# Kernel optimization log

Measured on AMD Instinct MI355X. Metric: run time of the kernel, lower is better.

## Reference

```python
import jax, jax.numpy as jnp
import numpy as np

H = 512  # hidden_dim
F = 512  # feat_vec_dim
N_LEAVES = 2048
BATCH = 8


def _tree_indices(n_leaves, batch_size):
    """Complete-binary-tree forest, nodes numbered bottom-up per tree:
    leaves 0..L-1, then L..L+L/2-1, ..., root last. Returns per-non-leaf-layer
    son/fa global index arrays (concatenated over the batch of trees)."""
    npt = 2 * n_leaves - 1  # nodes per tree
    levels = []
    start, size = 0, n_leaves
    while size >= 1:
        levels.append((start, size))
        start += size
        size //= 2
    offs = np.arange(batch_size) * npt
    def idx(l):
        s, sz = levels[l]
        return jnp.asarray((offs[:, None] + np.arange(s, s + sz)[None, :]).reshape(-1))
    n_layers = len(levels) - 1  # number of non-leaf layers (11 here)
    son = [idx(l) for l in range(n_layers)]
    fa = [idx(l + 1) for l in range(n_layers)]
    return son, fa, npt * batch_size, n_layers


def setup_inputs() -> dict:
    key = jax.random.key(0)
    ks = jax.random.split(key, 24)
    n_total = (2 * N_LEAVES - 1) * BATCH  # 32760
    s = 1.0 / np.sqrt(F)
    mk = lambda k: jax.random.normal(k, (H, F), dtype=jnp.float32) * s
    vk = lambda k: jax.random.normal(k, (H,), dtype=jnp.float32) * 0.02
    return {
        "feat_vec": jax.random.normal(ks[0], (n_total, F), dtype=jnp.float32),
        "Wh": mk(ks[1]), "Wz": mk(ks[2]), "Wr": mk(ks[3]),
        "Uh": mk(ks[4]), "Uz": mk(ks[5]), "bUz": vk(ks[6]),
        "Ur": mk(ks[7]), "bUr": vk(ks[8]),
        "Whd": mk(ks[9]), "Wzd": mk(ks[10]), "Wrd": mk(ks[11]),
        "Uhd": mk(ks[12]), "Uzd": mk(ks[13]), "bUzd": vk(ks[14]),
        "Urd": mk(ks[15]), "bUrd": vk(ks[16]),
        "W1": mk(ks[17]), "b1": jax.random.normal(ks[18], (F,), dtype=jnp.float32) * 0.02,
        "W2": mk(ks[19]), "b2": jax.random.normal(ks[20], (F,), dtype=jnp.float32) * 0.02,
        "n_leaves": N_LEAVES,
        "batch_size": BATCH,
    }


def reference(feat_vec, Wh, Wz, Wr, Uh, Uz, bUz, Ur, bUr,
              Whd, Wzd, Wrd, Uhd, Uzd, bUzd, Urd, bUrd,
              W1, b1, W2, b2, n_leaves, batch_size):
    son, fa, n_total, n_layers = _tree_indices(int(n_leaves), int(batch_size))
    sig, tanh = jax.nn.sigmoid, jnp.tanh

    # ---- bottom-up tree GRU ----
    h = jnp.zeros((n_total, H), dtype=feat_vec.dtype)
    # leaves: h = (1-z) * tanh(Wh x), z = sigmoid(Wz x)
    x0 = feat_vec[son[0]]
    z0 = sig(x0 @ Wz.T)
    h = h.at[son[0]].set((1.0 - z0) * tanh(x0 @ Wh.T))
    for l in range(n_layers):
        # A_T_sub @ h_son == sum of each father's two contiguous children
        h_son = h[son[l]]
        h_sum = h_son.reshape(-1, 2, H).sum(axis=1)
        x = feat_vec[fa[l]]
        z = sig(x @ Wz.T + h_sum @ Uz.T + bUz)
        r = sig(x @ Wr.T + h_sum @ Ur.T + bUr)
        cand = tanh(x @ Wh.T + (r * h_sum) @ Uh.T)
        h = h.at[fa[l]].set(z * h_sum + (1.0 - z) * cand)

    # ---- top-down tree GRU ----
    hd = jnp.zeros((n_total, H), dtype=feat_vec.dtype)
    roots = fa[n_layers - 1]
    hd = hd.at[roots].set(h[roots])
    for l in range(n_layers - 1, -1, -1):
        # A_sub @ hd_fa == each son gathers its (single) father's state
        h_fa = jnp.repeat(hd[fa[l]], 2, axis=0)
        x = feat_vec[son[l]]
        zd = sig(x @ Wzd.T + h_fa @ Uzd.T + bUzd)
        rd = sig(x @ Wrd.T + h_fa @ Urd.T + bUrd)
        cand = tanh(x @ Whd.T + (rd * h_fa) @ Uhd.T)
        hd = hd.at[son[l]].set(zd * h_fa + (1.0 - zd) * cand)

    # out = FFN1(h) + FFN2(hd)
    return h @ W1.T + b1 + hd @ W2.T + b2
```

## Files before the change

kernel.cpp:

```cpp
#include <hip/hip_runtime.h>
#include <hip/hip_bf16.h>
#include <cmath>
#include <cstdint>

#define NPT 4095
#define NT  32760
#define FD  512

using bf16 = __hip_bfloat16;
using bf8v = __attribute__((ext_vector_type(8))) short;
using us8v = __attribute__((ext_vector_type(8))) unsigned short;
using f4v  = __attribute__((ext_vector_type(4))) float;

__device__ __forceinline__ float b2f(bf16 x){ return __bfloat162float(x); }
__device__ __forceinline__ bf16  f2b(float x){ return __float2bfloat16(x); }
__device__ __forceinline__ float us2f(unsigned short u){ union{unsigned int i; float f;} v; v.i = ((unsigned)u)<<16; return v.f; }
__device__ __forceinline__ unsigned short f2us(float f){ union{bf16 b; unsigned short u;} v; v.b = __float2bfloat16(f); return v.u; }

__device__ __forceinline__ float fast_sig(float x){
  float e = __builtin_amdgcn_exp2f(-1.4426950408889634f * x);
  return __builtin_amdgcn_rcpf(1.f + e);
}
__device__ __forceinline__ float fast_tanh(float x){
  float ax = fabsf(x);
  float e = __builtin_amdgcn_exp2f(-2.885390081777927f * ax);
  float r = (1.f - e) * __builtin_amdgcn_rcpf(1.f + e);
  return copysignf(r, x);
}

__device__ __forceinline__ void gload_lds16(const bf16* g, bf16* l){
  __builtin_amdgcn_global_load_lds(
    (const __attribute__((address_space(1))) unsigned int*)g,
    (__attribute__((address_space(3))) unsigned int*)l, 16, 0, 0);
}


__global__ void cvt_b16(bf16* __restrict__ dst, const float* __restrict__ src, int n8){
  int e = blockIdx.x*256 + threadIdx.x;
  if (e >= n8) return;
  const float4* s = (const float4*)(src + (size_t)e*8);
  float4 a = s[0], b = s[1];
  us8v o = { f2us(a.x), f2us(a.y), f2us(a.z), f2us(a.w),
             f2us(b.x), f2us(b.y), f2us(b.z), f2us(b.w) };
  *(us8v*)(dst + (size_t)e*8) = o;
}

struct PackArgs { const float* s[16]; bf16* d[16]; int dk[16]; int ro[16]; int co[16]; };
__global__ void pack_all(PackArgs pa){
  int idx = blockIdx.x >> 7;
  int e = (blockIdx.x & 127)*256 + threadIdx.x;
  int r = e >> 6, c8 = e & 63;
  const float4* s = (const float4*)(pa.s[idx] + (size_t)r*512 + c8*8);
  float4 a = s[0], b = s[1];
  us8v o = { f2us(a.x), f2us(a.y), f2us(a.z), f2us(a.w),
             f2us(b.x), f2us(b.y), f2us(b.z), f2us(b.w) };
  *(us8v*)(pa.d[idx] + (size_t)(pa.ro[idx] + r)*pa.dk[idx] + pa.co[idx] + c8*8) = o;
}

__global__ void roots_k(bf16* __restrict__ hd, bf16* __restrict__ sA, const bf16* __restrict__ h){
  int e = blockIdx.x*256 + threadIdx.x;
  int t = e >> 6, c8 = e & 63;
  size_t off = ((size_t)t*NPT + 4094)*FD + c8*8;
  us8v v = *(const us8v*)(h + off);
  *(us8v*)(hd + off) = v;
  *(us8v*)(sA + (size_t)(2*t)*FD + c8*8) = v;
  *(us8v*)(sA + (size_t)(2*t+1)*FD + c8*8) = v;
}

__device__ __forceinline__ void epi4(
    const f4v& a, int rbase, int n, int M, int mode,
    const float* __restrict__ bias0, const float* __restrict__ bias1,
    const bf16* __restrict__ zb, const bf16* __restrict__ sb,
    const bf16* __restrict__ xw,
    bf16* __restrict__ o0, bf16* __restrict__ o1,
    bf16* __restrict__ hO, float* __restrict__ outF,
    int o_start, int o_log2, bf16* __restrict__ sN, int smode)
{
  if (rbase >= M) return;
  const int omask = (1 << o_log2) - 1;
  if (mode == 1){
    #pragma unroll
    for (int i = 0; i < 4; ++i){
      int row = rbase + i; if (row >= M) break;
      int tree = row >> o_log2, pos = row & omask;
      float v = a[i] + b2f(xw[((size_t)tree*NPT + o_start + pos)*1024 + n]);
      if (n < 512){
        o0[(size_t)row*FD + n] = f2b(fast_sig(v + bias0[n]));
      } else {
        float r = fast_sig(v + bias1[n-512]);
        size_t off = (size_t)row*FD + (n-512);
        o1[off] = f2b(r * b2f(sb[off]));
      }
    }
  } else {
    float hv[4];
    #pragma unroll
    for (int i = 0; i < 4; ++i){
      int row = rbase + i;
      if (row >= M){ hv[i] = 0.f; continue; }
      float c = fast_tanh(a[i]);
      size_t off = (size_t)row*FD + n;
      float z = b2f(zb[off]);
      float s = b2f(sb[off]);
      float h = z*s + (1.f - z)*c;
      hv[i] = h;
      int tree = row >> o_log2, pos = row & omask;
      hO[((size_t)tree*NPT + o_start + pos)*FD + n] = f2b(h);
    }
    if (smode == 1){
      if (rbase + 1 < M) sN[(size_t)(rbase>>1)*FD + n] = f2b(hv[0] + hv[1]);
      if (rbase + 3 < M) sN[(size_t)((rbase>>1) + 1)*FD + n] = f2b(hv[2] + hv[3]);
    } else if (smode == 2){
      #pragma unroll
      for (int i = 0; i < 4; ++i){
        int row = rbase + i; if (row >= M) break;
        bf16 hb = f2b(hv[i]);
        sN[(size_t)(2*row)*FD + n] = hb;
        sN[(size_t)(2*row+1)*FD + n] = hb;
      }
    }
  }
}

#define CPAD 132
__global__ __launch_bounds__(256) void gemm_big(
    const bf16* __restrict__ A0, const bf16* __restrict__ A1,
    const bf16* __restrict__ Wp, int M, int K, int ldb,
    int a_start, int a_log2, int o_start, int o_log2,
    const float* __restrict__ bias0, const float* __restrict__ bias1,
    const bf16* __restrict__ zb, const bf16* __restrict__ sb,
    const bf16* __restrict__ xw,
    bf16* __restrict__ o0, bf16* __restrict__ o1,
    bf16* __restrict__ hO, float* __restrict__ outF,
    bf16* __restrict__ sN, int smode, int mode)
{
  __shared__ __align__(16) char smemraw[64*CPAD*4];
  bf16* As = (bf16*)smemraw;
  bf16* Bs = As + 128*64;
  float* Cf = (float*)smemraw;

  const int t = threadIdx.x, lane = t & 63, wid = t >> 6;
  const int wr = wid >> 1, wc = wid & 1;
  const int lr = lane & 15, quad = lane >> 4;

  const int gx = gridDim.x, gy = gridDim.y;
  int nwg = gx * gy;
  int id = blockIdx.y * gx + blockIdx.x;
  int q = nwg >> 3, r8 = nwg & 7;
  int xcd = id & 7, jj = id >> 3;
  int wg = (xcd < r8 ? xcd*(q+1) : r8*(q+1) + (xcd - r8)*q) + jj;
  const int m_blk = (wg / gy) * 128, n_blk = (wg % gy) * 128;

  const int Mm1 = M - 1;
  const int amask = (1 << a_log2) - 1;
  const int wbase = (t & ~63);

  const bf16* a0p[4]; const bf16* a1p[4]; const bf16* bp[4];
  #pragma unroll
  for (int p = 0; p < 4; ++p){
    int c = p*256 + t;
    int rl = c >> 3, slot = c & 7;
    int g = slot ^ (rl & 7);
    int r = m_blk + rl; if (r > Mm1) r = Mm1;
    int tr = r >> a_log2, po = r & amask;
    a0p[p] = A0 + ((size_t)tr*NPT + a_start + po)*FD + g*8;
    a1p[p] = A1 + (size_t)r*FD + g*8;
    bp[p]  = Wp + (size_t)(n_blk + rl)*ldb + g*8;
  }

  f4v acc[4][4] = {};

  for (int k0 = 0; k0 < K; k0 += 64){
    #pragma unroll
    for (int p = 0; p < 4; ++p){
      const bf16* src = (k0 < 512) ? (a0p[p] + k0) : (a1p[p] + (k0 - 512));
      gload_lds16(src, &As[(size_t)(p*256 + wbase)*8]);
    }
    #pragma unroll
    for (int p = 0; p < 4; ++p)
      gload_lds16(bp[p] + k0, &Bs[(size_t)(p*256 + wbase)*8]);
    __syncthreads();

    #pragma unroll
    for (int kh = 0; kh < 2; ++kh){
      int cidx = kh*4 + quad;
      bf8v af[4], bv[4];
      #pragma unroll
      for (int i = 0; i < 4; ++i){
        int ra = wr*64 + i*16 + lr;
        af[i] = *(const bf8v*)&As[ra*64 + ((cidx ^ (ra & 7))*8)];
        int rb = wc*64 + i*16 + lr;
        bv[i] = *(const bf8v*)&Bs[rb*64 + ((cidx ^ (rb & 7))*8)];
      }
      #pragma unroll
      for (int i = 0; i < 4; ++i)
        #pragma unroll
        for (int j = 0; j < 4; ++j)
          acc[i][j] = __builtin_amdgcn_mfma_f32_16x16x32_bf16(af[i], bv[j], acc[i][j], 0, 0, 0);
    }
    __syncthreads();
  }

  const int omask = (1 << o_log2) - 1;
  const int L0 = (t >> 4) * 4;
  const int c0l = (t & 15) * 8;
  const int n0 = n_blk + c0l;
  const int grb0 = m_blk + (L0 >> 5)*64 + (L0 & 31);

  #define LOADV(i, vv) { float4 _v0 = *(const float4*)&Cf[(L0+(i))*CPAD + c0l]; \
                         float4 _v1 = *(const float4*)&Cf[(L0+(i))*CPAD + c0l + 4]; \
                         vv[0]=_v0.x; vv[1]=_v0.y; vv[2]=_v0.z; vv[3]=_v0.w; \
                         vv[4]=_v1.x; vv[5]=_v1.y; vv[6]=_v1.z; vv[7]=_v1.w; }

  #pragma unroll
  for (int p = 0; p < 2; ++p){
    __syncthreads();
    #pragma unroll
    for (int mt2 = 0; mt2 < 2; ++mt2){
      int lrow = wr*32 + mt2*16 + quad*4;
      #pragma unroll
      for (int nt = 0; nt < 4; ++nt){
        int c = wc*64 + nt*16 + lr;
        #pragma unroll
        for (int i = 0; i < 4; ++i)
          Cf[(lrow+i)*CPAD + c] = acc[2*p+mt2][nt][i];
      }
    }
    __syncthreads();

    const int gr = grb0 + p*32;

    if (mode == 3){
      #pragma unroll
      for (int i = 0; i < 4; ++i){
        int row = gr + i; if (row >= M) continue;
        float vv[8]; LOADV(i, vv);
        us8v o;
        #pragma unroll
        for (int k2 = 0; k2 < 8; ++k2) o[k2] = f2us(vv[k2]);
        *(us8v*)(o0 + (size_t)row*1024 + n0) = o;
      }
    } else if (mode == 4){
      float bb[8];
      *(float4*)&bb[0] = *(const float4*)&bias0[n0];
      *(float4*)&bb[4] = *(const float4*)&bias0[n0+4];
      float b2v[8];
      *(float4*)&b2v[0] = *(const float4*)&bias1[n0];
      *(float4*)&b2v[4] = *(const float4*)&bias1[n0+4];
      #pragma unroll
      for (int k2 = 0; k2 < 8; ++k2) bb[k2] += b2v[k2];
      #pragma unroll
      for (int i = 0; i < 4; ++i){
        int row = gr + i; if (row >= M) continue;
        float vv[8]; LOADV(i, vv);
        float4 o0v = { vv[0]+bb[0], vv[1]+bb[1], vv[2]+bb[2], vv[3]+bb[3] };
        float4 o1v = { vv[4]+bb[4], vv[5]+bb[5], vv[6]+bb[6], vv[7]+bb[7] };
        *(float4*)(outF + (size_t)row*FD + n0)     = o0v;
        *(float4*)(outF + (size_t)row*FD + n0 + 4) = o1v;
      }
    } else if (mode == 1){
      if (n0 < 512){
        float bb[8];
        *(float4*)&bb[0] = *(const float4*)&bias0[n0];
        *(float4*)&bb[4] = *(const float4*)&bias0[n0+4];
        #pragma unroll
        for (int i = 0; i < 4; ++i){
          int row = gr + i; if (row >= M) continue;
          size_t node = (size_t)(row >> o_log2)*NPT + o_start + (row & omask);
          us8v xv = *(const us8v*)(xw + node*1024 + n0);
          float vv[8]; LOADV(i, vv);
          us8v o;
          #pragma unroll
          for (int k2 = 0; k2 < 8; ++k2)
            o[k2] = f2us(fast_sig(vv[k2] + us2f(xv[k2]) + bb[k2]));
          *(us8v*)(o0 + (size_t)row*FD + n0) = o;
        }
      } else {
        int n5 = n0 - 512;
        float bb[8];
        *(float4*)&bb[0] = *(const float4*)&bias1[n5];
        *(float4*)&bb[4] = *(const float4*)&bias1[n5+4];
        #pragma unroll
        for (int i = 0; i < 4; ++i){
          int row = gr + i; if (row >= M) continue;
          size_t node = (size_t)(row >> o_log2)*NPT + o_start + (row & omask);
          us8v xv = *(const us8v*)(xw + node*1024 + n0);
          us8v sv = *(const us8v*)(sb + (size_t)row*FD + n5);
          float vv[8]; LOADV(i, vv);
          us8v o;
          #pragma unroll
          for (int k2 = 0; k2 < 8; ++k2){
            float r = fast_sig(vv[k2] + us2f(xv[k2]) + bb[k2]);
            o[k2] = f2us(r * us2f(sv[k2]));
          }
          *(us8v*)(o1 + (size_t)row*FD + n5) = o;
        }
      }
    } else if (mode == 5){
      float hprev[8];
      #pragma unroll
      for (int i = 0; i < 4; ++i){
        int row = gr + i; if (row >= M) continue;
        size_t node = (size_t)(row >> o_log2)*NPT + o_start + (row & omask);
        us8v zv = *(const us8v*)(xw + node*1024 + n0);
        float vv[8]; LOADV(i, vv);
        float hc[8]; us8v hb;
        #pragma unroll
        for (int k2 = 0; k2 < 8; ++k2){
          float h = (1.f - fast_sig(us2f(zv[k2]))) * fast_tanh(vv[k2]);
          hc[k2] = h; hb[k2] = f2us(h);
        }
        *(us8v*)(hO + node*FD + n0) = hb;
        if (i & 1){
          us8v ss;
          #pragma unroll
          for (int k2 = 0; k2 < 8; ++k2) ss[k2] = f2us(hprev[k2] + hc[k2]);
          *(us8v*)(sN + (size_t)(row>>1)*FD + n0) = ss;
        } else {
          #pragma unroll
          for (int k2 = 0; k2 < 8; ++k2) hprev[k2] = hc[k2];
        }
      }
    } else {
      float hprev[8];
      #pragma unroll
      for (int i = 0; i < 4; ++i){
        int row = gr + i; if (row >= M) continue;
        us8v zv = *(const us8v*)(zb + (size_t)row*FD + n0);
        us8v sv = *(const us8v*)(sb + (size_t)row*FD + n0);
        float vv[8]; LOADV(i, vv);
        float hc[8]; us8v hb;
        #pragma unroll
        for (int k2 = 0; k2 < 8; ++k2){
          float c = fast_tanh(vv[k2]);
          float z = us2f(zv[k2]);
          float s = us2f(sv[k2]);
          float h = z*s + (1.f - z)*c;
          hc[k2] = h; hb[k2] = f2us(h);
        }
        size_t node = (size_t)(row >> o_log2)*NPT + o_start + (row & omask);
        *(us8v*)(hO + node*FD + n0) = hb;
        if (smode == 1){
          if (i & 1){
            us8v ss;
            #pragma unroll
            for (int k2 = 0; k2 < 8; ++k2) ss[k2] = f2us(hprev[k2] + hc[k2]);
            *(us8v*)(sN + (size_t)(row>>1)*FD + n0) = ss;
          } else {
            #pragma unroll
            for (int k2 = 0; k2 < 8; ++k2) hprev[k2] = hc[k2];
          }
        } else if (smode == 2){
          *(us8v*)(sN + (size_t)(2*row)*FD + n0) = hb;
          *(us8v*)(sN + (size_t)(2*row+1)*FD + n0) = hb;
        }
      }
    }
  }
  #undef LOADV
}

__global__ __launch_bounds__(256) void gemm_small(
    const bf16* __restrict__ A0, const bf16* __restrict__ A1,
    const bf16* __restrict__ Wp, int M, int K, int ldb,
    int a_start, int a_log2, int o_start, int o_log2,
    const float* __restrict__ bias0, const float* __restrict__ bias1,
    const bf16* __restrict__ zb, const bf16* __restrict__ sb,
    const bf16* __restrict__ xw,
    bf16* __restrict__ o0, bf16* __restrict__ o1,
    bf16* __restrict__ hO, float* __restrict__ outF,
    bf16* __restrict__ sN, int smode, int mode)
{
  const int lane = threadIdx.x & 63, wid = threadIdx.x >> 6;
  const int wr = wid >> 1, wc = wid & 1;
  const int m_base = blockIdx.x*64 + wr*32;
  const int n_base = blockIdx.y*64 + wc*32;
  const int lr = lane & 15, quad = lane >> 4;
  const int Mm1 = M - 1;
  const int amask = (1 << a_log2) - 1;

  f4v acc[2][2] = {};

  const bf16 *a0p[2], *a1p[2], *bp[2];
  #pragma unroll
  for (int mt = 0; mt < 2; ++mt){
    int m = m_base + mt*16 + lr; if (m > Mm1) m = Mm1;
    int tr = m >> a_log2, po = m & amask;
    a0p[mt] = A0 + ((size_t)tr*NPT + a_start + po)*FD;
    a1p[mt] = A1 + (size_t)m*FD;
  }
  #pragma unroll
  for (int nt = 0; nt < 2; ++nt)
    bp[nt] = Wp + (size_t)(n_base + nt*16 + lr)*ldb;

  for (int k0 = 0; k0 < K; k0 += 32){
    int k = k0 + quad*8;
    bf8v a[2], b[2];
    #pragma unroll
    for (int mt = 0; mt < 2; ++mt)
      a[mt] = *(const bf8v*)((k0 < 512) ? (a0p[mt] + k) : (a1p[mt] + (k - 512)));
    #pragma unroll
    for (int nt = 0; nt < 2; ++nt)
      b[nt] = *(const bf8v*)(bp[nt] + k);
    #pragma unroll
    for (int mt = 0; mt < 2; ++mt)
      #pragma unroll
      for (int nt = 0; nt < 2; ++nt)
        acc[mt][nt] = __builtin_amdgcn_mfma_f32_16x16x32_bf16(a[mt], b[nt], acc[mt][nt], 0, 0, 0);
  }

  #pragma unroll
  for (int mt = 0; mt < 2; ++mt){
    int rbase = m_base + mt*16 + quad*4;
    #pragma unroll
    for (int nt = 0; nt < 2; ++nt){
      int n = n_base + nt*16 + lr;
      epi4(acc[mt][nt], rbase, n, M, mode, bias0, bias1, zb, sb, xw, o0, o1, hO, outF,
           o_start, o_log2, sN, smode);
    }
  }
}


extern "C" void kernel_launch(void* const* d_in, const int* in_sizes, int n_in,
                              void* d_out, int out_size, void* d_ws, size_t ws_size,
                              hipStream_t stream)
{
  const float* feat = (const float*)d_in[0];
  const float* Wh   = (const float*)d_in[1];
  const float* Wz   = (const float*)d_in[2];
  const float* Wr   = (const float*)d_in[3];
  const float* Uh   = (const float*)d_in[4];
  const float* Uz   = (const float*)d_in[5];
  const float* bUz  = (const float*)d_in[6];
  const float* Ur   = (const float*)d_in[7];
  const float* bUr  = (const float*)d_in[8];
  const float* Whd  = (const float*)d_in[9];
  const float* Wzd  = (const float*)d_in[10];
  const float* Wrd  = (const float*)d_in[11];
  const float* Uhd  = (const float*)d_in[12];
  const float* Uzd  = (const float*)d_in[13];
  const float* bUzd = (const float*)d_in[14];
  const float* Urd  = (const float*)d_in[15];
  const float* bUrd = (const float*)d_in[16];
  const float* W1   = (const float*)d_in[17];
  const float* b1   = (const float*)d_in[18];
  const float* W2   = (const float*)d_in[19];
  const float* b2   = (const float*)d_in[20];
  float* out = (float*)d_out;

  int starts[12], szs[12];
  { int s = 0, sz = 2048; for (int l = 0; l < 12; ++l){ starts[l] = s; szs[l] = sz; s += sz; sz >>= 1; } }

  char* p = (char*)d_ws;
  auto take = [&](size_t b)->char*{ char* q = p; p += (b + 255) & ~(size_t)255; return q; };
  bf16* featb = (bf16*)take((size_t)NT*FD*2);
  bf16* h_b   = (bf16*)take((size_t)NT*FD*2);
  bf16* hd_b  = (bf16*)take((size_t)NT*FD*2);
  bf16* Wzr_u = (bf16*)take((size_t)1024*512*2);
  bf16* Wzr_d = (bf16*)take((size_t)1024*512*2);
  bf16* Uzr_u = (bf16*)take((size_t)1024*512*2);
  bf16* Uzr_d = (bf16*)take((size_t)1024*512*2);
  bf16* Whu   = (bf16*)take((size_t)512*1024*2);
  bf16* Whu_d = (bf16*)take((size_t)512*1024*2);
  bf16* Wout  = (bf16*)take((size_t)512*1024*2);
  bf16* z16   = (bf16*)take((size_t)16384*512*2);
  bf16* rh16  = (bf16*)take((size_t)16384*512*2);
  bf16* sP0   = (bf16*)take((size_t)16384*512*2);
  bf16* sP1   = (bf16*)take((size_t)16384*512*2);
  if ((size_t)(p - (char*)d_ws) > ws_size) return;

  bf16* xWzr = (bf16*)d_out;

  cvt_b16<<<(NT*FD/8 + 255)/256, 256, 0, stream>>>(featb, feat, NT*FD/8);
  PackArgs pa;
  int pi = 0;
  auto pk = [&](const float* src, bf16* dst, int dk, int ro, int co){
    pa.s[pi] = src; pa.d[pi] = dst; pa.dk[pi] = dk; pa.ro[pi] = ro; pa.co[pi] = co; ++pi;
  };
  pk(Wz, Wzr_u, 512, 0, 0);    pk(Wr, Wzr_u, 512, 512, 0);
  pk(Wzd, Wzr_d, 512, 0, 0);   pk(Wrd, Wzr_d, 512, 512, 0);
  pk(Uz, Uzr_u, 512, 0, 0);    pk(Ur, Uzr_u, 512, 512, 0);
  pk(Uzd, Uzr_d, 512, 0, 0);   pk(Urd, Uzr_d, 512, 512, 0);
  pk(Wh, Whu, 1024, 0, 0);     pk(Uh, Whu, 1024, 0, 512);
  pk(Whd, Whu_d, 1024, 0, 0);  pk(Uhd, Whu_d, 1024, 0, 512);
  pk(W1, Wout, 1024, 0, 0);    pk(W2, Wout, 1024, 0, 512);
  pack_all<<<14*128, 256, 0, stream>>>(pa);

  auto gemm = [&](const bf16* A0, const bf16* A1, const bf16* Wp, int M, int N, int K, int ldb,
                  int a_start, int a_log2, int o_start, int o_log2,
                  const float* bias0, const float* bias1,
                  const bf16* zb, const bf16* sb, const bf16* xw,
                  bf16* o0, bf16* o1, bf16* hO, float* outF,
                  bf16* sN, int smode, int mode){
    if (M >= 2048){
      dim3 g((M + 127)/128, N/128);
      gemm_big<<<g, 256, 0, stream>>>(A0, A1, Wp, M, K, ldb, a_start, a_log2, o_start, o_log2,
                                      bias0, bias1, zb, sb, xw, o0, o1, hO, outF, sN, smode, mode);
    } else {
      dim3 g((M + 63)/64, N/64);
      gemm_small<<<g, 256, 0, stream>>>(A0, A1, Wp, M, K, ldb, a_start, a_log2, o_start, o_log2,
                                        bias0, bias1, zb, sb, xw, o0, o1, hO, outF, sN, smode, mode);
    }
  };

  gemm(featb, featb, Wzr_u, NT, 1024, 512, 512, 0, 26, 0, 26,
       nullptr, nullptr, nullptr, nullptr, nullptr, xWzr, nullptr, nullptr, nullptr, nullptr, 0, 3);

  gemm(featb, featb, Whu, 16384, 512, 512, 1024, 0, 11, 0, 11,
       nullptr, nullptr, nullptr, nullptr, xWzr, nullptr, nullptr, h_b, nullptr, sP0, 1, 5);

  for (int l = 0; l < 11; ++l){
    int Mf = 8*szs[l+1];
    int al2 = 10 - l, os = starts[l+1];
    bf16* sCur = (l & 1) ? sP1 : sP0;
    bf16* sNext = (l & 1) ? sP0 : sP1;
    int smode = (l < 10) ? 1 : 0;
    gemm(sCur, sCur, Uzr_u, Mf, 1024, 512, 512, 0, 26, os, al2,
         bUz, bUr, nullptr, sCur, xWzr, z16, rh16, nullptr, nullptr, nullptr, 0, 1);
    gemm(featb, rh16, Whu, Mf, 512, 1024, 1024, os, al2, os, al2,
         nullptr, nullptr, z16, sCur, nullptr, nullptr, nullptr, h_b, nullptr, sNext, smode, 2);
  }

  gemm(featb, featb, Wzr_d, NT, 1024, 512, 512, 0, 26, 0, 26,
       nullptr, nullptr, nullptr, nullptr, nullptr, xWzr, nullptr, nullptr, nullptr, nullptr, 0, 3);

  roots_k<<<2, 256, 0, stream>>>(hd_b, sP0, h_b);

  for (int l = 10; l >= 0; --l){
    int Ms = 8*szs[l];
    int al2 = 11 - l, os = starts[l];
    bf16* sCur = ((10 - l) & 1) ? sP1 : sP0;
    bf16* sNext = ((10 - l) & 1) ? sP0 : sP1;
    int smode = (l > 0) ? 2 : 0;
    gemm(sCur, sCur, Uzr_d, Ms, 1024, 512, 512, 0, 26, os, al2,
         bUzd, bUrd, nullptr, sCur, xWzr, z16, rh16, nullptr, nullptr, nullptr, 0, 1);
    gemm(featb, rh16, Whu_d, Ms, 512, 1024, 1024, os, al2, os, al2,
         nullptr, nullptr, z16, sCur, nullptr, nullptr, nullptr, hd_b, nullptr, sNext, smode, 2);
  }

  gemm(h_b, hd_b, Wout, NT, 512, 1024, 1024, 0, 26, 0, 26,
       b1, b2, nullptr, nullptr, nullptr, nullptr, nullptr, nullptr, out, nullptr, 0, 4);
}
```

Before: 1.154 ms.

## Fuse small tree levels into persistent cooperative kernel with grid sync

Replaces the per-level pairs of small GEMM launches for the upper tree levels (levels 3-10 bottom-up and 10-4 top-down) with one cooperative persistent kernel per direction. The kernel loops over levels, runs 64x64 tiles in a grid-strided way, and uses grid.sync between the gate GEMM and the candidate GEMM. The GEMM tile body is moved into a shared device function. This removes many tiny launches and their latency, at the cost of grid-wide barriers and a fixed 256-block grid that may underuse the GPU on some levels.

```diff
diff --git a/kernel.cpp b/kernel.cpp
--- a/kernel.cpp
+++ b/kernel.cpp
@@ -1,7 +1,10 @@
 #include <hip/hip_runtime.h>
+#include <hip/hip_cooperative_groups.h>
 #include <hip/hip_bf16.h>
 #include <cmath>
 #include <cstdint>
+
+namespace cg = cooperative_groups;
 
 #define NPT 4095
 #define NT  32760
@@ -119,6 +122,116 @@
         sN[(size_t)(2*row+1)*FD + n] = hb;
       }
     }
+  }
+}
+
+__device__ __forceinline__ void gemm64_tile(
+    int bx, int by,
+    const bf16* __restrict__ A0, const bf16* __restrict__ A1,
+    const bf16* __restrict__ Wp, int M, int K, int ldb,
+    int a_start, int a_log2, int o_start, int o_log2,
+    const float* __restrict__ bias0, const float* __restrict__ bias1,
+    const bf16* __restrict__ zb, const bf16* __restrict__ sb,
+    const bf16* __restrict__ xw,
+    bf16* __restrict__ o0, bf16* __restrict__ o1,
+    bf16* __restrict__ hO, float* __restrict__ outF,
+    bf16* __restrict__ sN, int smode, int mode)
+{
+  const int lane = threadIdx.x & 63, wid = threadIdx.x >> 6;
+  const int wr = wid >> 1, wc = wid & 1;
+  const int m_base = bx*64 + wr*32;
+  const int n_base = by*64 + wc*32;
+  const int lr = lane & 15, quad = lane >> 4;
+  const int Mm1 = M - 1;
+  const int amask = (1 << a_log2) - 1;
+
+  f4v acc[2][2] = {};
+
+  const bf16 *a0p[2], *a1p[2], *bp[2];
+  #pragma unroll
+  for (int mt = 0; mt < 2; ++mt){
+    int m = m_base + mt*16 + lr; if (m > Mm1) m = Mm1;
+    int tr = m >> a_log2, po = m & amask;
+    a0p[mt] = A0 + ((size_t)tr*NPT + a_start + po)*FD;
+    a1p[mt] = A1 + (size_t)m*FD;
+  }
+  #pragma unroll
+  for (int nt = 0; nt < 2; ++nt)
+    bp[nt] = Wp + (size_t)(n_base + nt*16 + lr)*ldb;
+
+  for (int k0 = 0; k0 < K; k0 += 32){
+    int k = k0 + quad*8;
+    bf8v a[2], b[2];
+    #pragma unroll
+    for (int mt = 0; mt < 2; ++mt)
+      a[mt] = *(const bf8v*)((k0 < 512) ? (a0p[mt] + k) : (a1p[mt] + (k - 512)));
+    #pragma unroll
+    for (int nt = 0; nt < 2; ++nt)
+      b[nt] = *(const bf8v*)(bp[nt] + k);
+    #pragma unroll
+    for (int mt = 0; mt < 2; ++mt)
+      #pragma unroll
+      for (int nt = 0; nt < 2; ++nt)
+        acc[mt][nt] = __builtin_amdgcn_mfma_f32_16x16x32_bf16(a[mt], b[nt], acc[mt][nt], 0, 0, 0);
+  }
+
+  #pragma unroll
+  for (int mt = 0; mt < 2; ++mt){
+    int rbase = m_base + mt*16 + quad*4;
+    #pragma unroll
+    for (int nt = 0; nt < 2; ++nt){
+      int n = n_base + nt*16 + lr;
+      epi4(acc[mt][nt], rbase, n, M, mode, bias0, bias1, zb, sb, xw, o0, o1, hO, outF,
+           o_start, o_log2, sN, smode);
+    }
+  }
+}
+
+__global__ __launch_bounds__(256) void tree_coop(
+    int dir,
+    const bf16* __restrict__ featb, const bf16* __restrict__ Uzr,
+    const bf16* __restrict__ Whu,
+    const float* __restrict__ bz, const float* __restrict__ br,
+    bf16* __restrict__ z16, bf16* __restrict__ rh16,
+    bf16* __restrict__ sP0, bf16* __restrict__ sP1,
+    const bf16* __restrict__ xw, bf16* __restrict__ hB)
+{
+  cg::grid_group g = cg::this_grid();
+  const int nb = gridDim.x;
+
+  int lbeg = (dir == 0) ? 3 : 10;
+  int lend = (dir == 0) ? 11 : 3;
+  int lstep = (dir == 0) ? 1 : -1;
+
+  for (int l = lbeg; l != lend; l += lstep){
+    int M, al2, os, par, smode;
+    if (dir == 0){
+      M = 8*(2048 >> (l+1));
+      al2 = 10 - l;
+      os = 4096 - (4096 >> (l+1));
+      par = l & 1;
+      smode = (l < 10) ? 1 : 0;
+    } else {
+      M = 8*(2048 >> l);
+      al2 = 11 - l;
+      os = 4096 - (4096 >> l);
+      par = (10 - l) & 1;
+      smode = 2;
+    }
+    bf16* sCur = par ? sP1 : sP0;
+    bf16* sNext = par ? sP0 : sP1;
+    int tm = (M + 63) >> 6;
+
+    for (int t = blockIdx.x; t < tm*16; t += nb)
+      gemm64_tile(t % tm, t / tm, sCur, sCur, Uzr, M, 512, 512, 0, 26, os, al2,
+                  bz, br, nullptr, sCur, xw, z16, rh16, nullptr, nullptr, nullptr, 0, 1);
+    __threadfence(); g.sync();
+
+    for (int t = blockIdx.x; t < tm*8; t += nb)
+      gemm64_tile(t % tm, t / tm, featb, rh16, Whu, M, 1024, 1024, os, al2, os, al2,
+                  nullptr, nullptr, z16, sCur, nullptr, nullptr, nullptr, hB, nullptr,
+                  sNext, smode, 2);
+    __threadfence(); g.sync();
   }
 }
 
@@ -371,54 +484,8 @@
     bf16* __restrict__ hO, float* __restrict__ outF,
     bf16* __restrict__ sN, int smode, int mode)
 {
-  const int lane = threadIdx.x & 63, wid = threadIdx.x >> 6;
-  const int wr = wid >> 1, wc = wid & 1;
-  const int m_base = blockIdx.x*64 + wr*32;
-  const int n_base = blockIdx.y*64 + wc*32;
-  const int lr = lane & 15, quad = lane >> 4;
-  const int Mm1 = M - 1;
-  const int amask = (1 << a_log2) - 1;
-
-  f4v acc[2][2] = {};
-
-  const bf16 *a0p[2], *a1p[2], *bp[2];
-  #pragma unroll
-  for (int mt = 0; mt < 2; ++mt){
-    int m = m_base + mt*16 + lr; if (m > Mm1) m = Mm1;
-    int tr = m >> a_log2, po = m & amask;
-    a0p[mt] = A0 + ((size_t)tr*NPT + a_start + po)*FD;
-    a1p[mt] = A1 + (size_t)m*FD;
-  }
-  #pragma unroll
-  for (int nt = 0; nt < 2; ++nt)
-    bp[nt] = Wp + (size_t)(n_base + nt*16 + lr)*ldb;
-
-  for (int k0 = 0; k0 < K; k0 += 32){
-    int k = k0 + quad*8;
-    bf8v a[2], b[2];
-    #pragma unroll
-    for (int mt = 0; mt < 2; ++mt)
-      a[mt] = *(const bf8v*)((k0 < 512) ? (a0p[mt] + k) : (a1p[mt] + (k - 512)));
-    #pragma unroll
-    for (int nt = 0; nt < 2; ++nt)
-      b[nt] = *(const bf8v*)(bp[nt] + k);
-    #pragma unroll
-    for (int mt = 0; mt < 2; ++mt)
-      #pragma unroll
-      for (int nt = 0; nt < 2; ++nt)
-        acc[mt][nt] = __builtin_amdgcn_mfma_f32_16x16x32_bf16(a[mt], b[nt], acc[mt][nt], 0, 0, 0);
-  }
-
-  #pragma unroll
-  for (int mt = 0; mt < 2; ++mt){
-    int rbase = m_base + mt*16 + quad*4;
-    #pragma unroll
-    for (int nt = 0; nt < 2; ++nt){
-      int n = n_base + nt*16 + lr;
-      epi4(acc[mt][nt], rbase, n, M, mode, bias0, bias1, zb, sb, xw, o0, o1, hO, outF,
-           o_start, o_log2, sN, smode);
-    }
-  }
+  gemm64_tile(blockIdx.x, blockIdx.y, A0, A1, Wp, M, K, ldb, a_start, a_log2,
+              o_start, o_log2, bias0, bias1, zb, sb, xw, o0, o1, hO, outF, sN, smode, mode);
 }
 
 
@@ -510,24 +577,44 @@
   gemm(featb, featb, Whu, 16384, 512, 512, 1024, 0, 11, 0, 11,
        nullptr, nullptr, nullptr, nullptr, xWzr, nullptr, nullptr, h_b, nullptr, sP0, 1, 5);
 
-  for (int l = 0; l < 11; ++l){
+  for (int l = 0; l < 3; ++l){
     int Mf = 8*szs[l+1];
     int al2 = 10 - l, os = starts[l+1];
     bf16* sCur = (l & 1) ? sP1 : sP0;
     bf16* sNext = (l & 1) ? sP0 : sP1;
-    int smode = (l < 10) ? 1 : 0;
+    int smode = 1;
     gemm(sCur, sCur, Uzr_u, Mf, 1024, 512, 512, 0, 26, os, al2,
          bUz, bUr, nullptr, sCur, xWzr, z16, rh16, nullptr, nullptr, nullptr, 0, 1);
     gemm(featb, rh16, Whu, Mf, 512, 1024, 1024, os, al2, os, al2,
          nullptr, nullptr, z16, sCur, nullptr, nullptr, nullptr, h_b, nullptr, sNext, smode, 2);
   }
 
+  {
+    int dir = 0;
+    const bf16 *a_featb = featb, *a_Uzr = Uzr_u, *a_Whu = Whu, *a_xw = xWzr;
+    const float *a_bz = bUz, *a_br = bUr;
+    bf16 *a_z = z16, *a_rh = rh16, *a_s0 = sP0, *a_s1 = sP1, *a_h = h_b;
+    void* args[] = { &dir, &a_featb, &a_Uzr, &a_Whu, &a_bz, &a_br,
+                     &a_z, &a_rh, &a_s0, &a_s1, &a_xw, &a_h };
+    hipLaunchCooperativeKernel((const void*)tree_coop, dim3(256), dim3(256), args, 0, stream);
+  }
+
   gemm(featb, featb, Wzr_d, NT, 1024, 512, 512, 0, 26, 0, 26,
        nullptr, nullptr, nullptr, nullptr, nullptr, xWzr, nullptr, nullptr, nullptr, nullptr, 0, 3);
 
   roots_k<<<2, 256, 0, stream>>>(hd_b, sP0, h_b);
 
-  for (int l = 10; l >= 0; --l){
+  {
+    int dir = 1;
+    const bf16 *a_featb = featb, *a_Uzr = Uzr_d, *a_Whu = Whu_d, *a_xw = xWzr;
+    const float *a_bz = bUzd, *a_br = bUrd;
+    bf16 *a_z = z16, *a_rh = rh16, *a_s0 = sP0, *a_s1 = sP1, *a_h = hd_b;
+    void* args[] = { &dir, &a_featb, &a_Uzr, &a_Whu, &a_bz, &a_br,
+                     &a_z, &a_rh, &a_s0, &a_s1, &a_xw, &a_h };
+    hipLaunchCooperativeKernel((const void*)tree_coop, dim3(256), dim3(256), args, 0, stream);
+  }
+
+  for (int l = 3; l >= 0; --l){
     int Ms = 8*szs[l];
     int al2 = 11 - l, os = starts[l];
     bf16* sCur = ((10 - l) & 1) ? sP1 : sP0;
```

Result: slower. 2.626 ms (+127.5%).

## Fuse gate and candidate GEMMs into one kernel for small tree levels

Applied to the files above, without the earlier changes.

For levels with fewer than 2048 rows, a new level_fused kernel replaces the two gemm_small launches per level. It computes the z gate, computes the full r*h row block into shared memory, then runs the candidate GEMM reading r*h from LDS. This removes one launch and the global round-trip of z and r*h per small level. In exchange, each block recomputes the full 512-column r gate GEMM redundantly across the 8 column blocks and holds 64KB of LDS, which limits occupancy.

```diff
diff --git a/kernel.cpp b/kernel.cpp
--- a/kernel.cpp
+++ b/kernel.cpp
@@ -67,56 +67,183 @@
   *(us8v*)(sA + (size_t)(2*t+1)*FD + c8*8) = v;
 }
 
-__device__ __forceinline__ void epi4(
-    const f4v& a, int rbase, int n, int M, int mode,
-    const float* __restrict__ bias0, const float* __restrict__ bias1,
-    const bf16* __restrict__ zb, const bf16* __restrict__ sb,
+__global__ __launch_bounds__(256) void level_fused(
+    const bf16* __restrict__ sCur, const bf16* __restrict__ featb,
+    const bf16* __restrict__ Uzr, const bf16* __restrict__ Whu,
+    const float* __restrict__ bz, const float* __restrict__ br,
     const bf16* __restrict__ xw,
-    bf16* __restrict__ o0, bf16* __restrict__ o1,
-    bf16* __restrict__ hO, float* __restrict__ outF,
-    int o_start, int o_log2, bf16* __restrict__ sN, int smode)
+    bf16* __restrict__ hO, bf16* __restrict__ sN,
+    int M, int o_start, int o_log2, int smode)
 {
-  if (rbase >= M) return;
+  __shared__ bf16 rhL[64*512];
+  const int t = threadIdx.x, lane = t & 63, wid = t >> 6;
+  const int lr = lane & 15, quad = lane >> 4;
+  const int wr = wid >> 1, wc = wid & 1;
+  const int m_base = blockIdx.x*64;
+  const int n_base = blockIdx.y*64;
+  const int Mm1 = M - 1;
   const int omask = (1 << o_log2) - 1;
-  if (mode == 1){
-    #pragma unroll
-    for (int i = 0; i < 4; ++i){
-      int row = rbase + i; if (row >= M) break;
-      int tree = row >> o_log2, pos = row & omask;
-      float v = a[i] + b2f(xw[((size_t)tree*NPT + o_start + pos)*1024 + n]);
-      if (n < 512){
-        o0[(size_t)row*FD + n] = f2b(fast_sig(v + bias0[n]));
-      } else {
-        float r = fast_sig(v + bias1[n-512]);
-        size_t off = (size_t)row*FD + (n-512);
-        o1[off] = f2b(r * b2f(sb[off]));
-      }
-    }
-  } else {
-    float hv[4];
-    #pragma unroll
-    for (int i = 0; i < 4; ++i){
-      int row = rbase + i;
-      if (row >= M){ hv[i] = 0.f; continue; }
-      float c = fast_tanh(a[i]);
-      size_t off = (size_t)row*FD + n;
-      float z = b2f(zb[off]);
-      float s = b2f(sb[off]);
-      float h = z*s + (1.f - z)*c;
-      hv[i] = h;
-      int tree = row >> o_log2, pos = row & omask;
-      hO[((size_t)tree*NPT + o_start + pos)*FD + n] = f2b(h);
-    }
-    if (smode == 1){
-      if (rbase + 1 < M) sN[(size_t)(rbase>>1)*FD + n] = f2b(hv[0] + hv[1]);
-      if (rbase + 3 < M) sN[(size_t)((rbase>>1) + 1)*FD + n] = f2b(hv[2] + hv[3]);
-    } else if (smode == 2){
+
+  f4v zac[2][2] = {};
+  {
+    const bf16 *ap[2], *bp[2];
+    #pragma unroll
+    for (int mt = 0; mt < 2; ++mt){
+      int m = m_base + wr*32 + mt*16 + lr; if (m > Mm1) m = Mm1;
+      ap[mt] = sCur + (size_t)m*FD + quad*8;
+    }
+    #pragma unroll
+    for (int nt = 0; nt < 2; ++nt)
+      bp[nt] = Uzr + (size_t)(n_base + wc*32 + nt*16 + lr)*512 + quad*8;
+    #pragma unroll 4
+    for (int k0 = 0; k0 < 512; k0 += 32){
+      bf8v a[2], b[2];
+      a[0] = *(const bf8v*)(ap[0] + k0); a[1] = *(const bf8v*)(ap[1] + k0);
+      b[0] = *(const bf8v*)(bp[0] + k0); b[1] = *(const bf8v*)(bp[1] + k0);
+      #pragma unroll
+      for (int mt = 0; mt < 2; ++mt)
+        #pragma unroll
+        for (int nt = 0; nt < 2; ++nt)
+          zac[mt][nt] = __builtin_amdgcn_mfma_f32_16x16x32_bf16(a[mt], b[nt], zac[mt][nt], 0, 0, 0);
+    }
+  }
+  f4v zv[2][2];
+  #pragma unroll
+  for (int mt = 0; mt < 2; ++mt){
+    int rbase = m_base + wr*32 + mt*16 + quad*4;
+    #pragma unroll
+    for (int nt = 0; nt < 2; ++nt){
+      int n = n_base + wc*32 + nt*16 + lr;
       #pragma unroll
       for (int i = 0; i < 4; ++i){
-        int row = rbase + i; if (row >= M) break;
-        bf16 hb = f2b(hv[i]);
-        sN[(size_t)(2*row)*FD + n] = hb;
-        sN[(size_t)(2*row+1)*FD + n] = hb;
+        int row = rbase + i; if (row > Mm1) row = Mm1;
+        size_t node = (size_t)(row >> o_log2)*NPT + o_start + (row & omask);
+        zv[mt][nt][i] = fast_sig(zac[mt][nt][i] + b2f(xw[node*1024 + n]) + bz[n]);
+      }
+    }
+  }
+
+  for (int cc = 0; cc < 2; ++cc){
+    int colb = wid*128 + cc*64;
+    f4v rac[4][4] = {};
+    const bf16 *ap[4], *bp[4];
+    #pragma unroll
+    for (int mt = 0; mt < 4; ++mt){
+      int m = m_base + mt*16 + lr; if (m > Mm1) m = Mm1;
+      ap[mt] = sCur + (size_t)m*FD + quad*8;
+    }
+    #pragma unroll
+    for (int nt = 0; nt < 4; ++nt)
+      bp[nt] = Uzr + (size_t)(512 + colb + nt*16 + lr)*512 + quad*8;
+    #pragma unroll 2
+    for (int k0 = 0; k0 < 512; k0 += 32){
+      bf8v a[4], b[4];
+      #pragma unroll
+      for (int mt = 0; mt < 4; ++mt) a[mt] = *(const bf8v*)(ap[mt] + k0);
+      #pragma unroll
+      for (int nt = 0; nt < 4; ++nt) b[nt] = *(const bf8v*)(bp[nt] + k0);
+      #pragma unroll
+      for (int mt = 0; mt < 4; ++mt)
+        #pragma unroll
+        for (int nt = 0; nt < 4; ++nt)
+          rac[mt][nt] = __builtin_amdgcn_mfma_f32_16x16x32_bf16(a[mt], b[nt], rac[mt][nt], 0, 0, 0);
+    }
+    #pragma unroll
+    for (int mt = 0; mt < 4; ++mt){
+      int rl0 = mt*16 + quad*4;
+      #pragma unroll
+      for (int nt = 0; nt < 4; ++nt){
+        int col = colb + nt*16 + lr;
+        #pragma unroll
+        for (int i = 0; i < 4; ++i){
+          int rl = rl0 + i;
+          int row = m_base + rl; if (row > Mm1) row = Mm1;
+          size_t node = (size_t)(row >> o_log2)*NPT + o_start + (row & omask);
+          float r = fast_sig(rac[mt][nt][i] + b2f(xw[node*1024 + 512 + col]) + br[col]);
+          float sv = b2f(sCur[(size_t)row*FD + col]);
+          int slot = (col >> 3) ^ (rl & 7);
+          rhL[rl*512 + slot*8 + (col & 7)] = f2b(r * sv);
+        }
+      }
+    }
+  }
+  __syncthreads();
+
+  f4v cac[2][2] = {};
+  {
+    const bf16 *ap[2], *bp[2];
+    int rla[2];
+    #pragma unroll
+    for (int mt = 0; mt < 2; ++mt){
+      int rl = wr*32 + mt*16 + lr;
+      rla[mt] = rl;
+      int m = m_base + rl; if (m > Mm1) m = Mm1;
+      size_t node = (size_t)(m >> o_log2)*NPT + o_start + (m & omask);
+      ap[mt] = featb + node*FD + quad*8;
+    }
+    #pragma unroll
+    for (int nt = 0; nt < 2; ++nt)
+      bp[nt] = Whu + (size_t)(n_base + wc*32 + nt*16 + lr)*1024 + quad*8;
+    #pragma unroll 4
+    for (int k0 = 0; k0 < 512; k0 += 32){
+      bf8v a[2], b[2];
+      a[0] = *(const bf8v*)(ap[0] + k0); a[1] = *(const bf8v*)(ap[1] + k0);
+      b[0] = *(const bf8v*)(bp[0] + k0); b[1] = *(const bf8v*)(bp[1] + k0);
+      #pragma unroll
+      for (int mt = 0; mt < 2; ++mt)
+        #pragma unroll
+        for (int nt = 0; nt < 2; ++nt)
+          cac[mt][nt] = __builtin_amdgcn_mfma_f32_16x16x32_bf16(a[mt], b[nt], cac[mt][nt], 0, 0, 0);
+    }
+    #pragma unroll 4
+    for (int k0 = 512; k0 < 1024; k0 += 32){
+      int chunk = ((k0 - 512) >> 3) + quad;
+      bf8v a[2], b[2];
+      #pragma unroll
+      for (int mt = 0; mt < 2; ++mt){
+        int slot = chunk ^ (rla[mt] & 7);
+        a[mt] = *(const bf8v*)&rhL[rla[mt]*512 + slot*8];
+      }
+      b[0] = *(const bf8v*)(bp[0] + k0); b[1] = *(const bf8v*)(bp[1] + k0);
+      #pragma unroll
+      for (int mt = 0; mt < 2; ++mt)
+        #pragma unroll
+        for (int nt = 0; nt < 2; ++nt)
+          cac[mt][nt] = __builtin_amdgcn_mfma_f32_16x16x32_bf16(a[mt], b[nt], cac[mt][nt], 0, 0, 0);
+    }
+  }
+
+  #pragma unroll
+  for (int mt = 0; mt < 2; ++mt){
+    int rbase = m_base + wr*32 + mt*16 + quad*4;
+    if (rbase >= M) continue;
+    #pragma unroll
+    for (int nt = 0; nt < 2; ++nt){
+      int n = n_base + wc*32 + nt*16 + lr;
+      float hv[4];
+      #pragma unroll
+      for (int i = 0; i < 4; ++i){
+        int row = rbase + i;
+        if (row >= M){ hv[i] = 0.f; continue; }
+        float c = fast_tanh(cac[mt][nt][i]);
+        float z = zv[mt][nt][i];
+        float s = b2f(sCur[(size_t)row*FD + n]);
+        float h = z*s + (1.f - z)*c;
+        hv[i] = h;
+        size_t node = (size_t)(row >> o_log2)*NPT + o_start + (row & omask);
+        hO[node*FD + n] = f2b(h);
+      }
+      if (smode == 1){
+        if (rbase + 1 < M) sN[(size_t)(rbase>>1)*FD + n] = f2b(hv[0] + hv[1]);
+        if (rbase + 3 < M) sN[(size_t)((rbase>>1)+1)*FD + n] = f2b(hv[2] + hv[3]);
+      } else if (smode == 2){
+        #pragma unroll
+        for (int i = 0; i < 4; ++i){
+          int row = rbase + i; if (row >= M) break;
+          bf16 hb = f2b(hv[i]);
+          sN[(size_t)(2*row)*FD + n] = hb;
+          sN[(size_t)(2*row+1)*FD + n] = hb;
+        }
       }
     }
   }
@@ -358,67 +485,6 @@
     }
   }
   #undef LOADV
-}
-
-__global__ __launch_bounds__(256) void gemm_small(
-    const bf16* __restrict__ A0, const bf16* __restrict__ A1,
-    const bf16* __restrict__ Wp, int M, int K, int ldb,
-    int a_start, int a_log2, int o_start, int o_log2,
-    const float* __restrict__ bias0, const float* __restrict__ bias1,
-    const bf16* __restrict__ zb, const bf16* __restrict__ sb,
-    const bf16* __restrict__ xw,
-    bf16* __restrict__ o0, bf16* __restrict__ o1,
-    bf16* __restrict__ hO, float* __restrict__ outF,
-    bf16* __restrict__ sN, int smode, int mode)
-{
-  const int lane = threadIdx.x & 63, wid = threadIdx.x >> 6;
-  const int wr = wid >> 1, wc = wid & 1;
-  const int m_base = blockIdx.x*64 + wr*32;
-  const int n_base = blockIdx.y*64 + wc*32;
-  const int lr = lane & 15, quad = lane >> 4;
-  const int Mm1 = M - 1;
-  const int amask = (1 << a_log2) - 1;
-
-  f4v acc[2][2] = {};
-
-  const bf16 *a0p[2], *a1p[2], *bp[2];
-  #pragma unroll
-  for (int mt = 0; mt < 2; ++mt){
-    int m = m_base + mt*16 + lr; if (m > Mm1) m = Mm1;
-    int tr = m >> a_log2, po = m & amask;
-    a0p[mt] = A0 + ((size_t)tr*NPT + a_start + po)*FD;
-    a1p[mt] = A1 + (size_t)m*FD;
-  }
-  #pragma unroll
-  for (int nt = 0; nt < 2; ++nt)
-    bp[nt] = Wp + (size_t)(n_base + nt*16 + lr)*ldb;
-
-  for (int k0 = 0; k0 < K; k0 += 32){
-    int k = k0 + quad*8;
-    bf8v a[2], b[2];
-    #pragma unroll
-    for (int mt = 0; mt < 2; ++mt)
-      a[mt] = *(const bf8v*)((k0 < 512) ? (a0p[mt] + k) : (a1p[mt] + (k - 512)));
-    #pragma unroll
-    for (int nt = 0; nt < 2; ++nt)
-      b[nt] = *(const bf8v*)(bp[nt] + k);
-    #pragma unroll
-    for (int mt = 0; mt < 2; ++mt)
-      #pragma unroll
-      for (int nt = 0; nt < 2; ++nt)
-        acc[mt][nt] = __builtin_amdgcn_mfma_f32_16x16x32_bf16(a[mt], b[nt], acc[mt][nt], 0, 0, 0);
-  }
-
-  #pragma unroll
-  for (int mt = 0; mt < 2; ++mt){
-    int rbase = m_base + mt*16 + quad*4;
-    #pragma unroll
-    for (int nt = 0; nt < 2; ++nt){
-      int n = n_base + nt*16 + lr;
-      epi4(acc[mt][nt], rbase, n, M, mode, bias0, bias1, zb, sb, xw, o0, o1, hO, outF,
-           o_start, o_log2, sN, smode);
-    }
-  }
 }
 
 
@@ -493,15 +559,9 @@
                   const bf16* zb, const bf16* sb, const bf16* xw,
                   bf16* o0, bf16* o1, bf16* hO, float* outF,
                   bf16* sN, int smode, int mode){
-    if (M >= 2048){
-      dim3 g((M + 127)/128, N/128);
-      gemm_big<<<g, 256, 0, stream>>>(A0, A1, Wp, M, K, ldb, a_start, a_log2, o_start, o_log2,
-                                      bias0, bias1, zb, sb, xw, o0, o1, hO, outF, sN, smode, mode);
-    } else {
-      dim3 g((M + 63)/64, N/64);
-      gemm_small<<<g, 256, 0, stream>>>(A0, A1, Wp, M, K, ldb, a_start, a_log2, o_start, o_log2,
-                                        bias0, bias1, zb, sb, xw, o0, o1, hO, outF, sN, smode, mode);
-    }
+    dim3 g((M + 127)/128, N/128);
+    gemm_big<<<g, 256, 0, stream>>>(A0, A1, Wp, M, K, ldb, a_start, a_log2, o_start, o_log2,
+                                    bias0, bias1, zb, sb, xw, o0, o1, hO, outF, sN, smode, mode);
   };
 
   gemm(featb, featb, Wzr_u, NT, 1024, 512, 512, 0, 26, 0, 26,
@@ -516,10 +576,16 @@
     bf16* sCur = (l & 1) ? sP1 : sP0;
     bf16* sNext = (l & 1) ? sP0 : sP1;
     int smode = (l < 10) ? 1 : 0;
-    gemm(sCur, sCur, Uzr_u, Mf, 1024, 512, 512, 0, 26, os, al2,
-         bUz, bUr, nullptr, sCur, xWzr, z16, rh16, nullptr, nullptr, nullptr, 0, 1);
-    gemm(featb, rh16, Whu, Mf, 512, 1024, 1024, os, al2, os, al2,
-         nullptr, nullptr, z16, sCur, nullptr, nullptr, nullptr, h_b, nullptr, sNext, smode, 2);
+    if (Mf >= 2048){
+      gemm(sCur, sCur, Uzr_u, Mf, 1024, 512, 512, 0, 26, os, al2,
+           bUz, bUr, nullptr, sCur, xWzr, z16, rh16, nullptr, nullptr, nullptr, 0, 1);
+      gemm(featb, rh16, Whu, Mf, 512, 1024, 1024, os, al2, os, al2,
+           nullptr, nullptr, z16, sCur, nullptr, nullptr, nullptr, h_b, nullptr, sNext, smode, 2);
+    } else {
+      dim3 g((Mf + 63)/64, 8);
+      level_fused<<<g, 256, 0, stream>>>(sCur, featb, Uzr_u, Whu, bUz, bUr, xWzr,
+                                         h_b, sNext, Mf, os, al2, smode);
+    }
   }
 
   gemm(featb, featb, Wzr_d, NT, 1024, 512, 512, 0, 26, 0, 26,
@@ -533,10 +599,16 @@
     bf16* sCur = ((10 - l) & 1) ? sP1 : sP0;
     bf16* sNext = ((10 - l) & 1) ? sP0 : sP1;
     int smode = (l > 0) ? 2 : 0;
-    gemm(sCur, sCur, Uzr_d, Ms, 1024, 512, 512, 0, 26, os, al2,
-         bUzd, bUrd, nullptr, sCur, xWzr, z16, rh16, nullptr, nullptr, nullptr, 0, 1);
-    gemm(featb, rh16, Whu_d, Ms, 512, 1024, 1024, os, al2, os, al2,
-         nullptr, nullptr, z16, sCur, nullptr, nullptr, nullptr, hd_b, nullptr, sNext, smode, 2);
+    if (Ms >= 2048){
+      gemm(sCur, sCur, Uzr_d, Ms, 1024, 512, 512, 0, 26, os, al2,
+           bUzd, bUrd, nullptr, sCur, xWzr, z16, rh16, nullptr, nullptr, nullptr, 0, 1);
+      gemm(featb, rh16, Whu_d, Ms, 512, 1024, 1024, os, al2, os, al2,
+           nullptr, nullptr, z16, sCur, nullptr, nullptr, nullptr, hd_b, nullptr, sNext, smode, 2);
+    } else {
+      dim3 g((Ms + 63)/64, 8);
+      level_fused<<<g, 256, 0, stream>>>(sCur, featb, Uzr_d, Whu_d, bUzd, bUrd, xWzr,
+                                         hd_b, sNext, Ms, os, al2, smode);
+    }
   }
 
   gemm(h_b, hd_b, Wout, NT, 512, 1024, 1024, 0, 26, 0, 26,
```

After: 1.796 ms. +55.6%, slower.
